# Optimization experiments

Hardware: AMD Instinct MI355X
Metric: run time of the kernel (lower is better)

Reference implementation:

```python
import jax, jax.numpy as jnp
import numpy as np


def setup_inputs() -> dict:
    key = jax.random.key(0)
    kq, kk, kv = jax.random.split(key, 3)
    B, M, QT, KVT, H = 2, 16, 2048, 2048, 128
    q = jax.random.normal(kq, (B, M, QT, H), dtype=jnp.float32)
    k = jax.random.normal(kk, (B, M, KVT, H), dtype=jnp.float32)
    v = jax.random.normal(kv, (B, M, KVT, H), dtype=jnp.float32)
    return {"q": q, "k": k, "v": v}


def reference(q, k, v):
    # QKBmm: broadcast-multiply + sum == einsum contraction over H.
    # NOTE: original module applies NO 1/sqrt(H) scaling.
    score = jnp.einsum("bmqh,bmkh->bmqk", q, k)  # [B,M,QT,KVT]
    score = jax.nn.softmax(score, axis=-1)
    # SVBmm: broadcast-multiply + sum over KVT.
    out = jnp.einsum("bmqk,bmkh->bmqh", score, v)  # [B,M,QT,H]
    return out
```

## Files before the change

kernel.cpp:

```cpp
#include <hip/hip_runtime.h>
#include <hip/hip_bf16.h>
#include <math.h>


#define HD     128
#define QTL    2048
#define KVTL   2048
#define NHEAD  32
#define KVBLK  64
#define NKT    (KVTL / KVBLK)
#define QBLKB  256
#define TILE_BYTES 32768
#define WS_NEEDED ((size_t)NHEAD * NKT * TILE_BYTES)

using f32x4  = __attribute__((ext_vector_type(4))) float;
using f32x16 = __attribute__((ext_vector_type(16))) float;
using f16x8  = __attribute__((ext_vector_type(8))) _Float16;
using i32x2  = __attribute__((ext_vector_type(2))) int;
using i32x4  = __attribute__((ext_vector_type(4))) int;
using bf16x8 = __attribute__((ext_vector_type(8))) __bf16;
using bf16x4 = __attribute__((ext_vector_type(4))) __bf16;

#define NK_CHUNK (NHEAD * NKT * 64 * 16)
#define NV_CHUNK (NHEAD * NKT * 8 * 128)

__global__ __launch_bounds__(256) void sdpa_prep(const float* __restrict__ kg,
                                                 const float* __restrict__ vg,
                                                 char* __restrict__ ws)
{
    const int idx = blockIdx.x * 256 + threadIdx.x;
    if (idx < NK_CHUNK) {
        const int s    = idx & 15;
        const int r    = (idx >> 4) & 63;
        const int kt   = (idx >> 10) & 31;
        const int head = idx >> 15;
        const int c    = s ^ (r & 15);
        const float* src = kg + ((size_t)head * KVTL + kt * 64 + r) * HD + c * 8;
        float4 a = *(const float4*)src;
        float4 b = *(const float4*)(src + 4);
        f16x8 h8;
        h8[0] = (_Float16)a.x; h8[1] = (_Float16)a.y;
        h8[2] = (_Float16)a.z; h8[3] = (_Float16)a.w;
        h8[4] = (_Float16)b.x; h8[5] = (_Float16)b.y;
        h8[6] = (_Float16)b.z; h8[7] = (_Float16)b.w;
        char* base = ws + (size_t)(head * NKT + kt) * TILE_BYTES;
        *(f16x8*)(base + r * 256 + s * 16) = h8;
    } else if (idx < NK_CHUNK + NV_CHUNK) {
        const int j    = idx - NK_CHUNK;
        const int h    = j & 127;
        const int c    = (j >> 7) & 7;
        const int kt   = (j >> 10) & 31;
        const int head = j >> 15;
        const int rr   = h & 63;
        const int u    = h >> 6;
        const int s    = (u * 8 + c) ^ (rr & 15);
        const float* src = vg + ((size_t)head * KVTL + kt * 64 + c * 8) * HD + h;
        f16x8 o;
        #pragma unroll
        for (int i = 0; i < 8; ++i)
            o[i] = (_Float16)src[(size_t)i * HD];
        char* base = ws + (size_t)(head * NKT + kt) * TILE_BYTES;
        *(f16x8*)(base + 16384 + rr * 256 + s * 16) = o;
    }
}

__device__ __forceinline__ void stage_tile(const char* __restrict__ g,
                                           char* lds, int t)
{
    #pragma unroll
    for (int j = 0; j < 4; ++j) {
        __builtin_amdgcn_global_load_lds(
            (const __attribute__((address_space(1))) void*)(g + j * 8192 + t * 16),
            (__attribute__((address_space(3))) void*)(lds + j * 8192 + t * 16),
            16, 0, 0);
    }
}

__global__ __launch_bounds__(512, 1) void sdpa_fwd(const float* __restrict__ qg,
                                                   const char* __restrict__ ws,
                                                   float* __restrict__ og)
{
    const int head  = blockIdx.y;
    const int qblk  = blockIdx.x * QBLKB;
    const float* qh = qg + (size_t)head * QTL * HD;
    const char*  wh = ws + (size_t)head * NKT * TILE_BYTES;

    const int t  = threadIdx.x;
    const int wv = t >> 6;
    const int l  = t & 63;
    const int lq = l & 31;
    const int hi = l >> 5;
    const int lm = l & 15;

    __shared__ __align__(16) char arena[65536];

    f16x8 qf[8];
    {
        const float* qrow = qh + (size_t)(qblk + wv * 32 + lq) * HD;
        #pragma unroll
        for (int hs = 0; hs < 8; ++hs) {
            float4 a = *(const float4*)(qrow + hs * 16 + hi * 8);
            float4 b = *(const float4*)(qrow + hs * 16 + hi * 8 + 4);
            f16x8 f;
            f[0] = (_Float16)a.x; f[1] = (_Float16)a.y;
            f[2] = (_Float16)a.z; f[3] = (_Float16)a.w;
            f[4] = (_Float16)b.x; f[5] = (_Float16)b.y;
            f[6] = (_Float16)b.z; f[7] = (_Float16)b.w;
            qf[hs] = f;
        }
    }

    f32x16 acc_o[4];
    #pragma unroll
    for (int ht = 0; ht < 4; ++ht)
        #pragma unroll
        for (int r = 0; r < 16; ++r) acc_o[ht][r] = 0.f;

    float m = -INFINITY, ln = 0.f;
    const float LOG2E = 1.4426950408889634f;

    stage_tile(wh, arena, t);
    __syncthreads();

    for (int kt = 0; kt < NKT; ++kt) {
        const int cur = kt & 1;
        char* base = arena + cur * 32768;
        if (kt + 1 < NKT)
            stage_tile(wh + (size_t)(kt + 1) * TILE_BYTES, arena + (cur ^ 1) * 32768, t);

        f32x16 acc_s[2];
        __builtin_amdgcn_s_setprio(1);
        #pragma unroll
        for (int kk = 0; kk < 2; ++kk) {
            f32x16 acc;
            #pragma unroll
            for (int r = 0; r < 16; ++r) acc[r] = 0.f;
            #pragma unroll
            for (int hs = 0; hs < 8; ++hs) {
                const int off = (kk * 32 + lq) * 256 + (((hs * 2 + hi) ^ lm) * 16);
                f16x8 kf = *(const f16x8*)(base + off);
                acc = __builtin_amdgcn_mfma_f32_32x32x16_f16(kf, qf[hs], acc, 0, 0, 0);
            }
            acc_s[kk] = acc;
        }
        __builtin_amdgcn_s_setprio(0);

        float pm0 = -INFINITY, pm1 = -INFINITY, pm2 = -INFINITY, pm3 = -INFINITY;
        #pragma unroll
        for (int kk = 0; kk < 2; ++kk)
            #pragma unroll
            for (int r = 0; r < 16; r += 4) {
                pm0 = fmaxf(pm0, acc_s[kk][r + 0]);
                pm1 = fmaxf(pm1, acc_s[kk][r + 1]);
                pm2 = fmaxf(pm2, acc_s[kk][r + 2]);
                pm3 = fmaxf(pm3, acc_s[kk][r + 3]);
            }
        float pmax = fmaxf(fmaxf(pm0, pm1), fmaxf(pm2, pm3));
        pmax = fmaxf(pmax, __shfl_xor(pmax, 32));

        if (!__all(pmax <= m + 8.0f)) {
            const float mnew = fmaxf(m, pmax);
            const float sc   = exp2f((m - mnew) * LOG2E);
            m = mnew; ln *= sc;
            #pragma unroll
            for (int ht = 0; ht < 4; ++ht)
                #pragma unroll
                for (int r = 0; r < 16; ++r) acc_o[ht][r] *= sc;
        }

        i32x4 fr[4];
        #pragma unroll
        for (int kk = 0; kk < 2; ++kk) {
            float p[16];
            float s0 = 0.f, s1 = 0.f, s2 = 0.f, s3 = 0.f;
            #pragma unroll
            for (int r = 0; r < 16; r += 4) {
                p[r + 0] = exp2f((acc_s[kk][r + 0] - m) * LOG2E); s0 += p[r + 0];
                p[r + 1] = exp2f((acc_s[kk][r + 1] - m) * LOG2E); s1 += p[r + 1];
                p[r + 2] = exp2f((acc_s[kk][r + 2] - m) * LOG2E); s2 += p[r + 2];
                p[r + 3] = exp2f((acc_s[kk][r + 3] - m) * LOG2E); s3 += p[r + 3];
            }
            ln += (s0 + s1) + (s2 + s3);
            int t01 = __builtin_bit_cast(int, __builtin_amdgcn_cvt_pkrtz(p[0],  p[1]));
            int t23 = __builtin_bit_cast(int, __builtin_amdgcn_cvt_pkrtz(p[2],  p[3]));
            int t45 = __builtin_bit_cast(int, __builtin_amdgcn_cvt_pkrtz(p[4],  p[5]));
            int t67 = __builtin_bit_cast(int, __builtin_amdgcn_cvt_pkrtz(p[6],  p[7]));
            int t89 = __builtin_bit_cast(int, __builtin_amdgcn_cvt_pkrtz(p[8],  p[9]));
            int tAB = __builtin_bit_cast(int, __builtin_amdgcn_cvt_pkrtz(p[10], p[11]));
            int tCD = __builtin_bit_cast(int, __builtin_amdgcn_cvt_pkrtz(p[12], p[13]));
            int tEF = __builtin_bit_cast(int, __builtin_amdgcn_cvt_pkrtz(p[14], p[15]));
            i32x2 sw;
            sw = __builtin_amdgcn_permlane32_swap(t01, t45, false, false);
            fr[2*kk][0] = sw[0]; fr[2*kk][2] = sw[1];
            sw = __builtin_amdgcn_permlane32_swap(t23, t67, false, false);
            fr[2*kk][1] = sw[0]; fr[2*kk][3] = sw[1];
            sw = __builtin_amdgcn_permlane32_swap(t89, tCD, false, false);
            fr[2*kk+1][0] = sw[0]; fr[2*kk+1][2] = sw[1];
            sw = __builtin_amdgcn_permlane32_swap(tAB, tEF, false, false);
            fr[2*kk+1][1] = sw[0]; fr[2*kk+1][3] = sw[1];
        }

        const char* Vb = base + 16384;
        __builtin_amdgcn_s_setprio(1);
        #pragma unroll
        for (int ht = 0; ht < 4; ++ht) {
            #pragma unroll
            for (int ks = 0; ks < 4; ++ks) {
                const int off = ((ht & 1) * 32 + lq) * 256 +
                                ((((ht >> 1) * 8 + ks * 2 + hi) ^ lm) * 16);
                f16x8 vf = *(const f16x8*)(Vb + off);
                acc_o[ht] = __builtin_amdgcn_mfma_f32_32x32x16_f16(
                    vf, __builtin_bit_cast(f16x8, fr[ks]), acc_o[ht], 0, 0, 0);
            }
        }
        __builtin_amdgcn_s_setprio(0);

        __syncthreads();
    }

    ln += __shfl_xor(ln, 32);
    const float inv = 1.f / ln;
    const int qloc = wv * 32 + lq;

    #pragma unroll
    for (int half = 0; half < 2; ++half) {
        __syncthreads();
        if ((wv >> 2) == half) {
            const int lrow = qloc - half * 128;
            #pragma unroll
            for (int ht = 0; ht < 4; ++ht) {
                #pragma unroll
                for (int r = 0; r < 4; ++r) {
                    f32x4 v;
                    v[0] = acc_o[ht][4*r+0] * inv;
                    v[1] = acc_o[ht][4*r+1] * inv;
                    v[2] = acc_o[ht][4*r+2] * inv;
                    v[3] = acc_o[ht][4*r+3] * inv;
                    const int slot = ht * 8 + 2 * r + hi;
                    *(f32x4*)(arena + lrow * 512 + ((slot ^ lq) * 16)) = v;
                }
            }
        }
        __syncthreads();
        float* ob = og + (size_t)(head * QTL + qblk + half * 128) * HD;
        #pragma unroll
        for (int j = 0; j < 8; ++j) {
            const int n  = j * 512 + t;
            const int qr = n >> 5;
            const int sl = n & 31;
            f32x4 v = *(const f32x4*)(arena + qr * 512 + ((sl ^ (qr & 31)) * 16));
            *(f32x4*)(ob + (size_t)qr * HD + sl * 4) = v;
        }
    }
}

__global__ __launch_bounds__(256) void sdpa_fwd_v1(const float* __restrict__ qg,
                                                   const float* __restrict__ kg,
                                                   const float* __restrict__ vg,
                                                   float* __restrict__ og)
{
    const int head  = blockIdx.y;
    const int qbase = blockIdx.x * 64;
    const float* qh = qg + (size_t)head * QTL * HD;
    const float* kh = kg + (size_t)head * KVTL * HD;
    const float* vh = vg + (size_t)head * KVTL * HD;
    float*       oh = og + (size_t)head * QTL * HD;

    const int t  = threadIdx.x;
    const int wv = t >> 6;
    const int l  = t & 63;
    const int lr = l & 15;
    const int lg = l >> 4;

    __shared__ __bf16 Kth[32][HD + 8];
    __shared__ __bf16 Ktl[32][HD + 8];
    __shared__ __bf16 Vt[HD][32 + 8];
    __shared__ __bf16 Pw[4][16][32 + 8];

    bf16x8 qfh[4], qfl[4];
    {
        const float* qrow = qh + (size_t)(qbase + wv * 16 + lr) * HD;
        #pragma unroll
        for (int ks = 0; ks < 4; ++ks) {
            bf16x8 fh, fl;
            #pragma unroll
            for (int i = 0; i < 8; ++i) {
                float x = qrow[ks * 32 + lg * 8 + i];
                __bf16 h = (__bf16)x;
                fh[i] = h;
                fl[i] = (__bf16)(x - (float)h);
            }
            qfh[ks] = fh; qfl[ks] = fl;
        }
    }

    f32x4 acc_o[8];
    #pragma unroll
    for (int h8 = 0; h8 < 8; ++h8) acc_o[h8] = (f32x4){0.f, 0.f, 0.f, 0.f};
    float mrow[4], lrow[4];
    #pragma unroll
    for (int r = 0; r < 4; ++r) { mrow[r] = -INFINITY; lrow[r] = 0.f; }
    const float LOG2E = 1.4426950408889634f;

    for (int kt = 0; kt < 64; ++kt) {
        const float* kbase = kh + (size_t)kt * 32 * HD;
        const float* vbase = vh + (size_t)kt * 32 * HD;
        __syncthreads();
        #pragma unroll
        for (int j = 0; j < 4; ++j) {
            const int e   = (j * 256 + t) * 4;
            const int row = e >> 7;
            const int col = e & 127;
            float4 f = *(const float4*)(kbase + e);
            bf16x4 h4, l4;
            h4[0] = (__bf16)f.x; l4[0] = (__bf16)(f.x - (float)h4[0]);
            h4[1] = (__bf16)f.y; l4[1] = (__bf16)(f.y - (float)h4[1]);
            h4[2] = (__bf16)f.z; l4[2] = (__bf16)(f.z - (float)h4[2]);
            h4[3] = (__bf16)f.w; l4[3] = (__bf16)(f.w - (float)h4[3]);
            *(bf16x4*)&Kth[row][col] = h4;
            *(bf16x4*)&Ktl[row][col] = l4;
        }
        #pragma unroll
        for (int j = 0; j < 4; ++j) {
            const int n     = t & 127;
            const int strip = (t >> 7) + 2 * j;
            bf16x4 b4;
            #pragma unroll
            for (int i = 0; i < 4; ++i)
                b4[i] = (__bf16)vbase[(size_t)(4 * strip + i) * HD + n];
            *(bf16x4*)&Vt[n][4 * strip] = b4;
        }
        __syncthreads();

        f32x4 acc_s[2];
        #pragma unroll
        for (int nt = 0; nt < 2; ++nt) {
            acc_s[nt] = (f32x4){0.f, 0.f, 0.f, 0.f};
            #pragma unroll
            for (int ks = 0; ks < 4; ++ks) {
                bf16x8 kh8 = *(const bf16x8*)&Kth[nt * 16 + lr][ks * 32 + lg * 8];
                bf16x8 kl8 = *(const bf16x8*)&Ktl[nt * 16 + lr][ks * 32 + lg * 8];
                acc_s[nt] = __builtin_amdgcn_mfma_f32_16x16x32_bf16(qfh[ks], kh8, acc_s[nt], 0, 0, 0);
                acc_s[nt] = __builtin_amdgcn_mfma_f32_16x16x32_bf16(qfl[ks], kh8, acc_s[nt], 0, 0, 0);
                acc_s[nt] = __builtin_amdgcn_mfma_f32_16x16x32_bf16(qfh[ks], kl8, acc_s[nt], 0, 0, 0);
            }
        }
        float p[2][4];
        #pragma unroll
        for (int r = 0; r < 4; ++r) {
            float vm = fmaxf(acc_s[0][r], acc_s[1][r]);
            vm = fmaxf(vm, __shfl_xor(vm, 1));
            vm = fmaxf(vm, __shfl_xor(vm, 2));
            vm = fmaxf(vm, __shfl_xor(vm, 4));
            vm = fmaxf(vm, __shfl_xor(vm, 8));
            const float mnew  = fmaxf(mrow[r], vm);
            const float scale = exp2f((mrow[r] - mnew) * LOG2E);
            mrow[r] = mnew;
            float ps = 0.f;
            #pragma unroll
            for (int nt = 0; nt < 2; ++nt) {
                float pe = exp2f((acc_s[nt][r] - mnew) * LOG2E);
                p[nt][r] = pe; ps += pe;
            }
            lrow[r] = lrow[r] * scale + ps;
            #pragma unroll
            for (int h8 = 0; h8 < 8; ++h8) acc_o[h8][r] *= scale;
        }
        #pragma unroll
        for (int nt = 0; nt < 2; ++nt)
            #pragma unroll
            for (int r = 0; r < 4; ++r)
                Pw[wv][lg * 4 + r][nt * 16 + lr] = (__bf16)p[nt][r];
        bf16x8 pf = *(const bf16x8*)&Pw[wv][lr][lg * 8];
        #pragma unroll
        for (int h8 = 0; h8 < 8; ++h8) {
            bf16x8 vf = *(const bf16x8*)&Vt[h8 * 16 + lr][lg * 8];
            acc_o[h8] = __builtin_amdgcn_mfma_f32_16x16x32_bf16(pf, vf, acc_o[h8], 0, 0, 0);
        }
    }
    float invl[4];
    #pragma unroll
    for (int r = 0; r < 4; ++r) {
        float s = lrow[r];
        s += __shfl_xor(s, 1);
        s += __shfl_xor(s, 2);
        s += __shfl_xor(s, 4);
        s += __shfl_xor(s, 8);
        invl[r] = 1.f / s;
    }
    float* ob = oh + (size_t)(qbase + wv * 16) * HD;
    #pragma unroll
    for (int h8 = 0; h8 < 8; ++h8)
        #pragma unroll
        for (int r = 0; r < 4; ++r)
            ob[(size_t)(lg * 4 + r) * HD + h8 * 16 + lr] = acc_o[h8][r] * invl[r];
}

extern "C" void kernel_launch(void* const* d_in, const int* in_sizes, int n_in,
                              void* d_out, int out_size, void* d_ws, size_t ws_size,
                              hipStream_t stream) {
    const float* q = (const float*)d_in[0];
    const float* k = (const float*)d_in[1];
    const float* v = (const float*)d_in[2];
    float* out = (float*)d_out;

    if (ws_size >= WS_NEEDED) {
        char* ws = (char*)d_ws;
        const int total_chunks = NK_CHUNK + NV_CHUNK;
        sdpa_prep<<<total_chunks / 256, 256, 0, stream>>>(k, v, ws);
        dim3 grid(QTL / QBLKB, NHEAD, 1);
        sdpa_fwd<<<grid, dim3(512, 1, 1), 0, stream>>>(q, ws, out);
    } else {
        dim3 grid(QTL / 64, NHEAD, 1);
        sdpa_fwd_v1<<<grid, dim3(256, 1, 1), 0, stream>>>(q, k, v, out);
    }
}
```

Measured before the change: 114.8 us.

## Halve Q block to 256 threads, two blocks per CU, register-staged KV prefetch

```diff
diff --git a/kernel.cpp b/kernel.cpp
--- a/kernel.cpp
+++ b/kernel.cpp
@@ -9,7 +9,7 @@
 #define NHEAD  32
 #define KVBLK  64
 #define NKT    (KVTL / KVBLK)
-#define QBLKB  256
+#define QBLKB  128
 #define TILE_BYTES 32768
 #define WS_NEEDED ((size_t)NHEAD * NKT * TILE_BYTES)
 
@@ -64,19 +64,7 @@
     }
 }
 
-__device__ __forceinline__ void stage_tile(const char* __restrict__ g,
-                                           char* lds, int t)
-{
-    #pragma unroll
-    for (int j = 0; j < 4; ++j) {
-        __builtin_amdgcn_global_load_lds(
-            (const __attribute__((address_space(1))) void*)(g + j * 8192 + t * 16),
-            (__attribute__((address_space(3))) void*)(lds + j * 8192 + t * 16),
-            16, 0, 0);
-    }
-}
-
-__global__ __launch_bounds__(512, 1) void sdpa_fwd(const float* __restrict__ qg,
+__global__ __launch_bounds__(256, 2) void sdpa_fwd(const float* __restrict__ qg,
                                                    const char* __restrict__ ws,
                                                    float* __restrict__ og)
 {
@@ -119,14 +107,26 @@
     float m = -INFINITY, ln = 0.f;
     const float LOG2E = 1.4426950408889634f;
 
-    stage_tile(wh, arena, t);
+    i32x4 stg[8];
+
+    #pragma unroll
+    for (int j = 0; j < 8; ++j)
+        stg[j] = *(const i32x4*)(wh + j * 4096 + t * 16);
+    #pragma unroll
+    for (int j = 0; j < 8; ++j)
+        *(i32x4*)(arena + j * 4096 + t * 16) = stg[j];
     __syncthreads();
 
     for (int kt = 0; kt < NKT; ++kt) {
         const int cur = kt & 1;
-        char* base = arena + cur * 32768;
-        if (kt + 1 < NKT)
-            stage_tile(wh + (size_t)(kt + 1) * TILE_BYTES, arena + (cur ^ 1) * 32768, t);
+        const char* base = arena + cur * 32768;
+
+        if (kt + 1 < NKT) {
+            const char* g = wh + (size_t)(kt + 1) * TILE_BYTES;
+            #pragma unroll
+            for (int j = 0; j < 8; ++j)
+                stg[j] = *(const i32x4*)(g + j * 4096 + t * 16);
+        }
 
         f32x16 acc_s[2];
         __builtin_amdgcn_s_setprio(1);
@@ -215,37 +215,40 @@
         }
         __builtin_amdgcn_s_setprio(0);
 
+        if (kt + 1 < NKT) {
+            char* nbuf = arena + (cur ^ 1) * 32768;
+            #pragma unroll
+            for (int j = 0; j < 8; ++j)
+                *(i32x4*)(nbuf + j * 4096 + t * 16) = stg[j];
+        }
+
         __syncthreads();
     }
 
     ln += __shfl_xor(ln, 32);
     const float inv = 1.f / ln;
+
+    __syncthreads();
     const int qloc = wv * 32 + lq;
-
-    #pragma unroll
-    for (int half = 0; half < 2; ++half) {
-        __syncthreads();
-        if ((wv >> 2) == half) {
-            const int lrow = qloc - half * 128;
-            #pragma unroll
-            for (int ht = 0; ht < 4; ++ht) {
-                #pragma unroll
-                for (int r = 0; r < 4; ++r) {
-                    f32x4 v;
-                    v[0] = acc_o[ht][4*r+0] * inv;
-                    v[1] = acc_o[ht][4*r+1] * inv;
-                    v[2] = acc_o[ht][4*r+2] * inv;
-                    v[3] = acc_o[ht][4*r+3] * inv;
-                    const int slot = ht * 8 + 2 * r + hi;
-                    *(f32x4*)(arena + lrow * 512 + ((slot ^ lq) * 16)) = v;
-                }
-            }
-        }
-        __syncthreads();
-        float* ob = og + (size_t)(head * QTL + qblk + half * 128) * HD;
-        #pragma unroll
-        for (int j = 0; j < 8; ++j) {
-            const int n  = j * 512 + t;
+    #pragma unroll
+    for (int ht = 0; ht < 4; ++ht) {
+        #pragma unroll
+        for (int r = 0; r < 4; ++r) {
+            f32x4 v;
+            v[0] = acc_o[ht][4*r+0] * inv;
+            v[1] = acc_o[ht][4*r+1] * inv;
+            v[2] = acc_o[ht][4*r+2] * inv;
+            v[3] = acc_o[ht][4*r+3] * inv;
+            const int slot = ht * 8 + 2 * r + hi;
+            *(f32x4*)(arena + qloc * 512 + ((slot ^ lq) * 16)) = v;
+        }
+    }
+    __syncthreads();
+    {
+        float* ob = og + (size_t)(head * QTL + qblk) * HD;
+        #pragma unroll
+        for (int j = 0; j < 16; ++j) {
+            const int n  = j * 256 + t;
             const int qr = n >> 5;
             const int sl = n & 31;
             f32x4 v = *(const f32x4*)(arena + qr * 512 + ((sl ^ (qr & 31)) * 16));
@@ -409,7 +412,7 @@
         const int total_chunks = NK_CHUNK + NV_CHUNK;
         sdpa_prep<<<total_chunks / 256, 256, 0, stream>>>(k, v, ws);
         dim3 grid(QTL / QBLKB, NHEAD, 1);
-        sdpa_fwd<<<grid, dim3(512, 1, 1), 0, stream>>>(q, ws, out);
+        sdpa_fwd<<<grid, dim3(256, 1, 1), 0, stream>>>(q, ws, out);
     } else {
         dim3 grid(QTL / 64, NHEAD, 1);
         sdpa_fwd_v1<<<grid, dim3(256, 1, 1), 0, stream>>>(q, k, v, out);
```

New measurement: 115.9 us. Within noise of the previous version (+1.0%).
